# Kernel optimization log

Measured on AMD Instinct MI355X. Metric: run time of the kernel, lower is better.

## Reference

```python
import jax, jax.numpy as jnp
import numpy as np

# Config matching init_kwargs: input_shape=(C,T,H,W)=(512,32,14,14), window_size=9, n_heads=8
B, C, T, H, W = 2, 512, 32, 14, 14
N, K = 8, 9
CI = C // N              # per-head inter channels (64)
P = (K - 1) // 2         # symmetric temporal zero-pad so S == T


def setup_inputs() -> dict:
    key = jax.random.key(0)
    ks = jax.random.split(key, 7)
    s = 0.02
    return {
        "x":  jax.random.normal(ks[0], (B, C, T, H, W), jnp.float32),
        # per-head 1x1x1 conv (Linear3d) weights/biases, stacked over heads
        "Wq": jax.random.normal(ks[1], (N, CI, C), jnp.float32) * s,
        "bq": jax.random.normal(ks[2], (N, CI), jnp.float32) * s,
        "Wk": jax.random.normal(ks[3], (N, CI, C), jnp.float32) * s,
        "bk": jax.random.normal(ks[4], (N, CI), jnp.float32) * s,
        "Wv": jax.random.normal(ks[5], (N, CI, C), jnp.float32) * s,
        "bv": jax.random.normal(ks[6], (N, CI), jnp.float32) * s,
    }


def reference(x, Wq, bq, Wk, bk, Wv, bv):
    # x: (B, C, T, H, W). Dropout (p=0.25) is inference-mode identity.
    Bx, Cx, Tx, Hx, Wd = x.shape
    HW = Hx * Wd
    xf = x.reshape(Bx, Cx, Tx, HW)

    # Queries: every original frame is the center of its own window -> project x directly.
    q = jnp.einsum('bctp,nic->bnitp', xf, Wq) + bq[None, :, :, None, None]  # (B,N,ci,T,HW)

    # Keys/values on temporally zero-padded input (Pad3d gives S == T windows).
    xp = jnp.pad(xf, ((0, 0), (0, 0), (P, P), (0, 0)))  # (B,C,T+K-1,HW)
    k = jnp.einsum('bctp,nic->bnitp', xp, Wk) + bk[None, :, :, None, None]
    v = jnp.einsum('bctp,nic->bnitp', xp, Wv) + bv[None, :, :, None, None]

    # Sliding windows over padded time: window s covers padded frames s..s+K-1
    win = jnp.arange(Tx)[:, None] + jnp.arange(K)[None, :]  # (T,K)
    kw = k[:, :, :, win]  # (B,N,ci,T,K,HW)
    vw = v[:, :, :, win].reshape(Bx, N, CI, Tx, K * HW)

    # alpha[b,n,t,p,m] = sum_i q[b,n,i,t,p] * k_win[b,n,i,t,m]; softmax over keys m
    alpha = jnp.einsum('bnitp,bnitkm->bntpkm', q, kw).reshape(Bx, N, Tx, HW, K * HW)
    alpha = jax.nn.softmax(alpha, axis=-1)

    # y = alpha @ value -> (B,N,ci,T,HW); head concat is channel-major reshape
    y = jnp.einsum('bntpm,bnitm->bnitp', alpha, vw)
    z = y.reshape(Bx, Cx, Tx, Hx, Wd) + x  # residual
    return z
```

## Files before the change

### kernel.cpp

```cpp
#include <hip/hip_runtime.h>
#include <hip/hip_bf16.h>
#include <stdint.h>
#include <cstddef>

#define BB  2
#define CC  512
#define TT  32
#define HWP 196
#define NH  8
#define KWIN 9
#define CID 64
#define PPAD 4
#define TP  40
#define MTOT 12544
#define NTOT 1536
#define VSLOT 224
#define GPITCH 72
#define LOG2E 1.44269504f

typedef unsigned short u16;
typedef unsigned int   u32;
typedef __attribute__((ext_vector_type(8))) short short8;
typedef __attribute__((ext_vector_type(4))) float floatx4;

__device__ __forceinline__ u16 f2bf(float f) {
    u32 u = __float_as_uint(f);
    u32 r = (u + 0x7fffu + ((u >> 16) & 1u)) >> 16;
    return (u16)r;
}
__device__ __forceinline__ u32 pack2bf(float a, float b) {
    return (u32)f2bf(a) | ((u32)f2bf(b) << 16);
}
__device__ __forceinline__ u32 packtrunc(float a, float b) {
    return __builtin_amdgcn_perm(__float_as_uint(b), __float_as_uint(a), 0x07060302u);
}
__device__ __forceinline__ float fexp2(float x) {
    return __builtin_amdgcn_exp2f(x);
}

__global__ __launch_bounds__(256) void prep_misc(
    const float* __restrict__ Wq, const float* __restrict__ Wk,
    const float* __restrict__ Wv, u16* __restrict__ Wbf,
    const float* __restrict__ bk, const float* __restrict__ bv,
    u16* __restrict__ Kout, u16* __restrict__ Vtp)
{
    int id = blockIdx.x * 256 + threadIdx.x;
    const int wtot = NTOT * CC / 2;
    const int kper = 2 * NH * 8 * HWP * 32;
    const int vper = 2 * NH * 8 * 64 * (VSLOT/2);
    if (id < wtot) {
        int c2 = id & 255;
        int oc = id >> 8;
        int kind = oc >> 9;
        int idx = oc & 511;
        const float* src = (kind == 0 ? Wq : (kind == 1 ? Wk : Wv)) + (size_t)idx * CC + c2 * 2;
        ((u32*)Wbf)[id] = pack2bf(src[0], src[1]);
    } else if (id < wtot + kper) {
        int i = id - wtot;
        int ci2 = i & 31; i >>= 5;
        int p = i % HWP;  i /= HWP;
        int fr = i & 7;   i >>= 3;
        int head = i & 7;
        int b = i >> 3;
        int tp = fr < 4 ? fr : fr + 32;
        const float* bias = bk + head * CID + ci2 * 2;
        size_t addr = (((size_t)(b * NH + head) * TP + tp) * HWP + p) * 32 + ci2;
        ((u32*)Kout)[addr] = pack2bf(bias[0], bias[1]);
    } else if (id < wtot + kper + vper) {
        int i = id - wtot - kper;
        int s2 = i % (VSLOT/2); i /= (VSLOT/2);
        int ci = i & 63; i >>= 6;
        int fr = i & 7;  i >>= 3;
        int head = i & 7;
        int b = i >> 3;
        int tp = fr < 4 ? fr : fr + 32;
        float bias = bv[head * CID + ci];
        size_t addr = (((size_t)(b * NH + head) * TP + tp) * 64 + ci) * (VSLOT/2) + s2;
        ((u32*)Vtp)[addr] = pack2bf(bias, bias);
    }
}

__global__ __launch_bounds__(256) void transpose_x(
    const float* __restrict__ x, u16* __restrict__ xt)
{
    __shared__ float T[64 * 197];
    int bx = blockIdx.x;
    int ct = bx & 7; bx >>= 3;
    int t = bx & 31;
    int b = bx >> 5;
    int tid = threadIdx.x;
    const float* src = x + ((size_t)(b * CC + ct * 64) * TT + t) * HWP;
    for (int i = tid; i < 64 * HWP; i += 256) {
        int c = i / HWP;
        int p = i - c * HWP;
        T[c * 197 + p] = src[(size_t)c * (TT * HWP) + p];
    }
    __syncthreads();
    u16* dst = xt + (size_t)((b * TT + t) * HWP) * CC + ct * 64;
    for (int i = tid; i < HWP * 64; i += 256) {
        int p = i >> 6;
        int c = i & 63;
        dst[(size_t)p * CC + c] = f2bf(T[c * 197 + p]);
    }
}

__global__ __launch_bounds__(512) void proj_gemm2(
    const u16* __restrict__ xt, const u16* __restrict__ Wbf,
    const float* __restrict__ bq, const float* __restrict__ bk,
    const float* __restrict__ bv,
    u16* __restrict__ Qout, u16* __restrict__ Kout, u16* __restrict__ Vplain)
{
    __shared__ u16 sA[128 * GPITCH];
    __shared__ u16 sB[256 * GPITCH];

    int bx = blockIdx.x;
    int nb = bx % 6;
    int mt = bx / 6;
    int tid = threadIdx.x;
    int wave = tid >> 6, lane = tid & 63, quad = lane >> 4, l15 = lane & 15;
    int wm = wave >> 2, wn = wave & 3;
    int mbase = mt * 128 + wm * 64;
    int nbase = nb * 256 + wn * 64;

    floatx4 acc[4][4];
    #pragma unroll
    for (int ms = 0; ms < 4; ms++)
        #pragma unroll
        for (int ns = 0; ns < 4; ns++)
            acc[ms][ns] = (floatx4){0.f, 0.f, 0.f, 0.f};

    const u16* agbase = xt + (size_t)(mt * 128) * CC;
    const u16* bgbase = Wbf + (size_t)(nb * 256) * CC;

    for (int kc = 0; kc < 8; kc++) {
        __syncthreads();
        #pragma unroll
        for (int it = 0; it < 2; it++) {
            int idx = it * 512 + tid;
            int row = idx >> 3, jj = idx & 7;
            uint4 v = *(const uint4*)(agbase + (size_t)row * CC + kc * 64 + jj * 8);
            *(uint4*)&sA[row * GPITCH + jj * 8] = v;
        }
        #pragma unroll
        for (int it = 0; it < 4; it++) {
            int idx = it * 512 + tid;
            int row = idx >> 3, jj = idx & 7;
            uint4 v = *(const uint4*)(bgbase + (size_t)row * CC + kc * 64 + jj * 8);
            *(uint4*)&sB[row * GPITCH + jj * 8] = v;
        }
        __syncthreads();

        #pragma unroll
        for (int kk = 0; kk < 2; kk++) {
            short8 af[4], bf[4];
            #pragma unroll
            for (int ms = 0; ms < 4; ms++)
                af[ms] = *(const short8*)&sA[(wm * 64 + ms * 16 + l15) * GPITCH + kk * 32 + quad * 8];
            #pragma unroll
            for (int ns = 0; ns < 4; ns++)
                bf[ns] = *(const short8*)&sB[(wn * 64 + ns * 16 + l15) * GPITCH + kk * 32 + quad * 8];
            #pragma unroll
            for (int ms = 0; ms < 4; ms++)
                #pragma unroll
                for (int ns = 0; ns < 4; ns++)
                    acc[ms][ns] = __builtin_amdgcn_mfma_f32_16x16x32_bf16(
                        af[ms], bf[ns], acc[ms][ns], 0, 0, 0);
        }
    }

    float biasv[4];
    #pragma unroll
    for (int ns = 0; ns < 4; ns++) {
        int n = nbase + ns * 16 + l15;
        int kind = n >> 9;
        int idx = n & 511;
        const float* bpb = kind == 0 ? bq : (kind == 1 ? bk : bv);
        biasv[ns] = bpb[idx];
    }

    #pragma unroll
    for (int ms = 0; ms < 4; ms++) {
        #pragma unroll
        for (int r = 0; r < 4; r++) {
            int m = mbase + ms * 16 + quad * 4 + r;
            int b = m / (TT * HWP);
            int rem = m - b * (TT * HWP);
            int t = rem / HWP;
            int p = rem - t * HWP;
            #pragma unroll
            for (int ns = 0; ns < 4; ns++) {
                int n = nbase + ns * 16 + l15;
                int kind = n >> 9;
                int idx = n & 511;
                int head = idx >> 6;
                int ci = idx & 63;
                float val = acc[ms][ns][r] + biasv[ns];
                if (kind == 0) {
                    Qout[(((size_t)(b * NH + head) * TT + t) * HWP + p) * CID + ci]
                        = f2bf(val * LOG2E);
                } else if (kind == 1) {
                    Kout[(((size_t)(b * NH + head) * TP + (t + PPAD)) * HWP + p) * CID + ci]
                        = f2bf(val);
                } else {
                    Vplain[(((size_t)(b * NH + head) * TT + t) * HWP + p) * CID + ci]
                        = f2bf(val);
                }
            }
        }
    }
}

__global__ __launch_bounds__(256) void v_reformat(
    const u16* __restrict__ Vplain, u16* __restrict__ Vtp)
{
    __shared__ u16 T[HWP * 66];
    int bx = blockIdx.x;
    int t = bx & 31;
    int slab = bx >> 5;
    int tid = threadIdx.x;
    const u32* src = (const u32*)(Vplain + ((size_t)slab * TT + t) * (HWP * CID));
    for (int i = tid; i < HWP * 32; i += 256) {
        int p = i >> 5, c2 = i & 31;
        u32 v = src[i];
        T[p * 66 + c2 * 2]     = (u16)(v & 0xffffu);
        T[p * 66 + c2 * 2 + 1] = (u16)(v >> 16);
    }
    __syncthreads();
    u32* dst = (u32*)(Vtp + ((size_t)slab * TP + (t + PPAD)) * (64 * VSLOT));
    for (int i = tid; i < 64 * 98; i += 256) {
        int ci = i / 98;
        int s2 = i - ci * 98;
        int s = s2 * 2;
        int s5 = s & 31;
        int p0 = (s & ~31) | (((s5 >> 2) & 1) << 4) | ((s5 >> 3) << 2) | (s5 & 3);
        u32 lo = T[p0 * 66 + ci];
        u32 hi = T[(p0 + 1) * 66 + ci];
        dst[ci * (VSLOT / 2) + s2] = lo | (hi << 16);
    }
}

__global__ __launch_bounds__(256, 2) void attn_mfma4(
    const float* __restrict__ x,
    const u16* __restrict__ Qb, const u16* __restrict__ Kb,
    const u16* __restrict__ Vtp, float* __restrict__ zout)
{
    __shared__ float eT[HWP * 66];

    int i = blockIdx.x;
    int xcd = i & 7;
    int r = i >> 3;
    int slab = ((r >= 32) ? 8 : 0) | xcd;
    int t = r & 31;
    int b = slab >> 3, n = slab & 7;

    int tid = threadIdx.x;
    int wave = tid >> 6;
    int lane = tid & 63;
    int quad = lane >> 4, l15 = lane & 15;

    const u16* kfr0 = Kb + (size_t)slab * (TP * HWP) * CID;
    const u16* vslab = Vtp + (size_t)slab * (TP * 64 * VSLOT);
    const float tmask = (quad == 0) ? 1.0f : 0.0f;

    short8 qf[4][2];
    #pragma unroll
    for (int j = 0; j < 4; j++) {
        int qrow = (wave + 4 * j) * 16 + l15;
        qrow = qrow < HWP ? qrow : (HWP - 1);
        const u16* qp = Qb + ((size_t)(slab * TT + t) * HWP + qrow) * CID;
        qf[j][0] = *(const short8*)(qp + quad * 8);
        qf[j][1] = *(const short8*)(qp + 32 + quad * 8);
    }

    floatx4 acc[4][4];
    floatx4 accl[4];
    #pragma unroll
    for (int j = 0; j < 4; j++) {
        #pragma unroll
        for (int cg = 0; cg < 4; cg++) acc[j][cg] = (floatx4){0.f, 0.f, 0.f, 0.f};
        accl[j] = (floatx4){0.f, 0.f, 0.f, 0.f};
    }

    union { u32 w[4]; short8 s; } ones;
    ones.w[0] = 0x3F803F80u; ones.w[1] = 0x3F803F80u;
    ones.w[2] = 0x3F803F80u; ones.w[3] = 0x3F803F80u;

    #define KLOAD(c, D00, D01, D10, D11) do {                                    \
        const u16* a0_ = kfr0 + (size_t)(rbase + (c) * 32 + l15) * CID + quad * 8;\
        const u16* a1_ = a0_ + (size_t)16 * CID;                                 \
        D00 = *(const short8*)a0_;  D01 = *(const short8*)(a0_ + 32);            \
        D10 = *(const short8*)a1_;  D11 = *(const short8*)(a1_ + 32);            \
    } while (0)

    #define KLOADTAIL(D00, D01) do {                                             \
        int g_ = rbase + 192 + l15;                                              \
        g_ = g_ < (TP * HWP - 1) ? g_ : (TP * HWP - 1);                          \
        const u16* a0_ = kfr0 + (size_t)g_ * CID + quad * 8;                     \
        D00 = *(const short8*)a0_;  D01 = *(const short8*)(a0_ + 32);            \
    } while (0)

    #define VLOAD(c, D0, D1, D2, D3) do {                                        \
        const u16* v_ = vfr + l15 * VSLOT + (c) * 32 + quad * 8;                 \
        D0 = *(const short8*)v_;                                                 \
        D1 = *(const short8*)(v_ + 16 * VSLOT);                                  \
        D2 = *(const short8*)(v_ + 32 * VSLOT);                                  \
        D3 = *(const short8*)(v_ + 48 * VSLOT);                                  \
    } while (0)

    #define CHUNK_FULL(K00, K01, K10, K11, V0, V1, V2, V3)                       \
        _Pragma("unroll")                                                        \
        for (int j = 0; j < 4; j++) {                                            \
            floatx4 sc0 = (floatx4){0.f, 0.f, 0.f, 0.f};                         \
            sc0 = __builtin_amdgcn_mfma_f32_16x16x32_bf16(K00, qf[j][0], sc0, 0, 0, 0); \
            sc0 = __builtin_amdgcn_mfma_f32_16x16x32_bf16(K01, qf[j][1], sc0, 0, 0, 0); \
            floatx4 sc1 = (floatx4){0.f, 0.f, 0.f, 0.f};                         \
            sc1 = __builtin_amdgcn_mfma_f32_16x16x32_bf16(K10, qf[j][0], sc1, 0, 0, 0); \
            sc1 = __builtin_amdgcn_mfma_f32_16x16x32_bf16(K11, qf[j][1], sc1, 0, 0, 0); \
            union { u32 w[4]; short8 s; } pf;                                    \
            pf.w[0] = packtrunc(fexp2(sc0[0]), fexp2(sc0[1]));                   \
            pf.w[1] = packtrunc(fexp2(sc0[2]), fexp2(sc0[3]));                   \
            pf.w[2] = packtrunc(fexp2(sc1[0]), fexp2(sc1[1]));                   \
            pf.w[3] = packtrunc(fexp2(sc1[2]), fexp2(sc1[3]));                   \
            acc[j][0] = __builtin_amdgcn_mfma_f32_16x16x32_bf16(pf.s, V0, acc[j][0], 0, 0, 0); \
            acc[j][1] = __builtin_amdgcn_mfma_f32_16x16x32_bf16(pf.s, V1, acc[j][1], 0, 0, 0); \
            acc[j][2] = __builtin_amdgcn_mfma_f32_16x16x32_bf16(pf.s, V2, acc[j][2], 0, 0, 0); \
            acc[j][3] = __builtin_amdgcn_mfma_f32_16x16x32_bf16(pf.s, V3, acc[j][3], 0, 0, 0); \
            accl[j]   = __builtin_amdgcn_mfma_f32_16x16x32_bf16(pf.s, ones.s, accl[j], 0, 0, 0); \
        }

    #define CHUNK_TAIL(K00, K01, V0, V1, V2, V3)                                 \
        _Pragma("unroll")                                                        \
        for (int j = 0; j < 4; j++) {                                            \
            floatx4 sc0 = (floatx4){0.f, 0.f, 0.f, 0.f};                         \
            sc0 = __builtin_amdgcn_mfma_f32_16x16x32_bf16(K00, qf[j][0], sc0, 0, 0, 0); \
            sc0 = __builtin_amdgcn_mfma_f32_16x16x32_bf16(K01, qf[j][1], sc0, 0, 0, 0); \
            union { u32 w[4]; short8 s; } pf;                                    \
            pf.w[0] = packtrunc(fexp2(sc0[0]) * tmask, fexp2(sc0[1]) * tmask);   \
            pf.w[1] = packtrunc(fexp2(sc0[2]) * tmask, fexp2(sc0[3]) * tmask);   \
            pf.w[2] = 0u;                                                        \
            pf.w[3] = 0u;                                                        \
            acc[j][0] = __builtin_amdgcn_mfma_f32_16x16x32_bf16(pf.s, V0, acc[j][0], 0, 0, 0); \
            acc[j][1] = __builtin_amdgcn_mfma_f32_16x16x32_bf16(pf.s, V1, acc[j][1], 0, 0, 0); \
            acc[j][2] = __builtin_amdgcn_mfma_f32_16x16x32_bf16(pf.s, V2, acc[j][2], 0, 0, 0); \
            acc[j][3] = __builtin_amdgcn_mfma_f32_16x16x32_bf16(pf.s, V3, acc[j][3], 0, 0, 0); \
            accl[j]   = __builtin_amdgcn_mfma_f32_16x16x32_bf16(pf.s, ones.s, accl[j], 0, 0, 0); \
        }

    for (int f = 0; f < KWIN; f++) {
        int rbase = (t + f) * HWP;
        const u16* vfr = vslab + (size_t)(t + f) * (64 * VSLOT);

        short8 ka00, ka01, ka10, ka11, kb00, kb01, kb10, kb11;
        short8 va0, va1, va2, va3, vb0, vb1, vb2, vb3;

        KLOAD(0, ka00, ka01, ka10, ka11);  VLOAD(0, va0, va1, va2, va3);
        KLOAD(1, kb00, kb01, kb10, kb11);  VLOAD(1, vb0, vb1, vb2, vb3);
        CHUNK_FULL(ka00, ka01, ka10, ka11, va0, va1, va2, va3);
        KLOAD(2, ka00, ka01, ka10, ka11);  VLOAD(2, va0, va1, va2, va3);
        CHUNK_FULL(kb00, kb01, kb10, kb11, vb0, vb1, vb2, vb3);
        KLOAD(3, kb00, kb01, kb10, kb11);  VLOAD(3, vb0, vb1, vb2, vb3);
        CHUNK_FULL(ka00, ka01, ka10, ka11, va0, va1, va2, va3);
        KLOAD(4, ka00, ka01, ka10, ka11);  VLOAD(4, va0, va1, va2, va3);
        CHUNK_FULL(kb00, kb01, kb10, kb11, vb0, vb1, vb2, vb3);
        KLOAD(5, kb00, kb01, kb10, kb11);  VLOAD(5, vb0, vb1, vb2, vb3);
        CHUNK_FULL(ka00, ka01, ka10, ka11, va0, va1, va2, va3);
        KLOADTAIL(ka00, ka01);             VLOAD(6, va0, va1, va2, va3);
        CHUNK_FULL(kb00, kb01, kb10, kb11, vb0, vb1, vb2, vb3);
        CHUNK_TAIL(ka00, ka01, va0, va1, va2, va3);
    }

    #undef KLOAD
    #undef KLOADTAIL
    #undef VLOAD
    #undef CHUNK_FULL
    #undef CHUNK_TAIL

    #pragma unroll
    for (int j = 0; j < 4; j++) {
        int tg = wave + 4 * j;
        float il[4];
        #pragma unroll
        for (int rr = 0; rr < 4; rr++) il[rr] = 1.0f / accl[j][rr];
        #pragma unroll
        for (int cg = 0; cg < 4; cg++) {
            #pragma unroll
            for (int rr = 0; rr < 4; rr++) {
                int p = tg * 16 + quad * 4 + rr;
                if (p < HWP)
                    eT[p * 66 + cg * 16 + l15] = acc[j][cg][rr] * il[rr];
            }
        }
    }
    __syncthreads();

    if (tid < HWP) {
        size_t base = ((size_t)(b * CC + n * CID) * TT + t) * HWP + tid;
        for (int ci = 0; ci < 64; ci++) {
            size_t a = base + (size_t)ci * (TT * HWP);
            zout[a] = eT[tid * 66 + ci] + x[a];
        }
    }
}

extern "C" void kernel_launch(void* const* d_in, const int* in_sizes, int n_in,
                              void* d_out, int out_size, void* d_ws, size_t ws_size,
                              hipStream_t stream) {
    const float* x  = (const float*)d_in[0];
    const float* Wq = (const float*)d_in[1];
    const float* bq = (const float*)d_in[2];
    const float* Wk = (const float*)d_in[3];
    const float* bk = (const float*)d_in[4];
    const float* Wv = (const float*)d_in[5];
    const float* bv = (const float*)d_in[6];
    float* z = (float*)d_out;

    const size_t qElems   = (size_t)BB * NH * TT * HWP * CID;
    const size_t kElems   = (size_t)BB * NH * TP * HWP * CID;
    const size_t vtpElems = (size_t)BB * NH * TP * 64 * VSLOT;

    u16* Qw  = (u16*)d_ws;
    u16* Kw  = Qw + qElems;
    u16* Vtp = Kw + kElems;
    u16* Wb  = Vtp + vtpElems;
    u16* Xt  = (u16*)d_out;
    u16* Vpl = Xt + qElems;

    {
        const int wtot = NTOT * CC / 2;
        const int kper = 2 * NH * 8 * HWP * 32;
        const int vper = 2 * NH * 8 * 64 * (VSLOT / 2);
        prep_misc<<<(wtot + kper + vper + 255) / 256, 256, 0, stream>>>(
            Wq, Wk, Wv, Wb, bk, bv, Kw, Vtp);
    }
    transpose_x<<<BB * TT * 8, 256, 0, stream>>>(x, Xt);
    proj_gemm2<<<98 * 6, 512, 0, stream>>>(Xt, Wb, bq, bk, bv, Qw, Kw, Vpl);
    v_reformat<<<BB * NH * TT, 256, 0, stream>>>(Vpl, Vtp);
    attn_mfma4<<<512, 256, 0, stream>>>(x, Qw, Kw, Vtp, z);
}
```

Measured before the change: 254.5 us.

## Split attention query rows across two blocks and drop K/V double buffering

Each attention block now handles half of the 196 query positions (two 16-row tiles per wave instead of four), doubling the grid from 512 to 1024 blocks. The aim is better CU occupancy and lower per-thread register pressure. The manual ping-pong K/V register prefetch is replaced with a simple unrolled loop, and the output epilogue is spread across all 256 threads. In exchange, every K/V tile is now loaded by twice as many blocks, so K/V memory traffic doubles, and some load/compute overlap may be lost. The second half-block is partly wasted because 196 is not a multiple of 128.

After: 328.0 us. 28.9% more time.

```diff
diff --git a/kernel.cpp b/kernel.cpp
--- a/kernel.cpp
+++ b/kernel.cpp
@@ -244,13 +244,15 @@
     const u16* __restrict__ Qb, const u16* __restrict__ Kb,
     const u16* __restrict__ Vtp, float* __restrict__ zout)
 {
-    __shared__ float eT[HWP * 66];
+    __shared__ float eT[128 * 66];
 
     int i = blockIdx.x;
     int xcd = i & 7;
     int r = i >> 3;
-    int slab = ((r >= 32) ? 8 : 0) | xcd;
-    int t = r & 31;
+    int slab = ((r >= 64) ? 8 : 0) | xcd;
+    int rr = r & 63;
+    int t = rr >> 1;
+    int h = rr & 1;
     int b = slab >> 3, n = slab & 7;
 
     int tid = threadIdx.x;
@@ -262,20 +264,21 @@
     const u16* vslab = Vtp + (size_t)slab * (TP * 64 * VSLOT);
     const float tmask = (quad == 0) ? 1.0f : 0.0f;
 
-    short8 qf[4][2];
-    #pragma unroll
-    for (int j = 0; j < 4; j++) {
-        int qrow = (wave + 4 * j) * 16 + l15;
+    short8 qf[2][2];
+    #pragma unroll
+    for (int j = 0; j < 2; j++) {
+        int tg = 8 * h + wave + 4 * j;
+        int qrow = tg * 16 + l15;
         qrow = qrow < HWP ? qrow : (HWP - 1);
         const u16* qp = Qb + ((size_t)(slab * TT + t) * HWP + qrow) * CID;
         qf[j][0] = *(const short8*)(qp + quad * 8);
         qf[j][1] = *(const short8*)(qp + 32 + quad * 8);
     }
 
-    floatx4 acc[4][4];
-    floatx4 accl[4];
-    #pragma unroll
-    for (int j = 0; j < 4; j++) {
+    floatx4 acc[2][4];
+    floatx4 accl[2];
+    #pragma unroll
+    for (int j = 0; j < 2; j++) {
         #pragma unroll
         for (int cg = 0; cg < 4; cg++) acc[j][cg] = (floatx4){0.f, 0.f, 0.f, 0.f};
         accl[j] = (floatx4){0.f, 0.f, 0.f, 0.f};
@@ -309,7 +312,7 @@
 
     #define CHUNK_FULL(K00, K01, K10, K11, V0, V1, V2, V3)                       \
         _Pragma("unroll")                                                        \
-        for (int j = 0; j < 4; j++) {                                            \
+        for (int j = 0; j < 2; j++) {                                            \
             floatx4 sc0 = (floatx4){0.f, 0.f, 0.f, 0.f};                         \
             sc0 = __builtin_amdgcn_mfma_f32_16x16x32_bf16(K00, qf[j][0], sc0, 0, 0, 0); \
             sc0 = __builtin_amdgcn_mfma_f32_16x16x32_bf16(K01, qf[j][1], sc0, 0, 0, 0); \
@@ -330,7 +333,7 @@
 
     #define CHUNK_TAIL(K00, K01, V0, V1, V2, V3)                                 \
         _Pragma("unroll")                                                        \
-        for (int j = 0; j < 4; j++) {                                            \
+        for (int j = 0; j < 2; j++) {                                            \
             floatx4 sc0 = (floatx4){0.f, 0.f, 0.f, 0.f};                         \
             sc0 = __builtin_amdgcn_mfma_f32_16x16x32_bf16(K00, qf[j][0], sc0, 0, 0, 0); \
             sc0 = __builtin_amdgcn_mfma_f32_16x16x32_bf16(K01, qf[j][1], sc0, 0, 0, 0); \
@@ -350,23 +353,18 @@
         int rbase = (t + f) * HWP;
         const u16* vfr = vslab + (size_t)(t + f) * (64 * VSLOT);
 
-        short8 ka00, ka01, ka10, ka11, kb00, kb01, kb10, kb11;
-        short8 va0, va1, va2, va3, vb0, vb1, vb2, vb3;
-
-        KLOAD(0, ka00, ka01, ka10, ka11);  VLOAD(0, va0, va1, va2, va3);
-        KLOAD(1, kb00, kb01, kb10, kb11);  VLOAD(1, vb0, vb1, vb2, vb3);
-        CHUNK_FULL(ka00, ka01, ka10, ka11, va0, va1, va2, va3);
-        KLOAD(2, ka00, ka01, ka10, ka11);  VLOAD(2, va0, va1, va2, va3);
-        CHUNK_FULL(kb00, kb01, kb10, kb11, vb0, vb1, vb2, vb3);
-        KLOAD(3, kb00, kb01, kb10, kb11);  VLOAD(3, vb0, vb1, vb2, vb3);
-        CHUNK_FULL(ka00, ka01, ka10, ka11, va0, va1, va2, va3);
-        KLOAD(4, ka00, ka01, ka10, ka11);  VLOAD(4, va0, va1, va2, va3);
-        CHUNK_FULL(kb00, kb01, kb10, kb11, vb0, vb1, vb2, vb3);
-        KLOAD(5, kb00, kb01, kb10, kb11);  VLOAD(5, vb0, vb1, vb2, vb3);
-        CHUNK_FULL(ka00, ka01, ka10, ka11, va0, va1, va2, va3);
-        KLOADTAIL(ka00, ka01);             VLOAD(6, va0, va1, va2, va3);
-        CHUNK_FULL(kb00, kb01, kb10, kb11, vb0, vb1, vb2, vb3);
-        CHUNK_TAIL(ka00, ka01, va0, va1, va2, va3);
+        short8 k00, k01, k10, k11;
+        short8 v0, v1, v2, v3;
+
+        #pragma unroll
+        for (int c = 0; c < 6; c++) {
+            KLOAD(c, k00, k01, k10, k11);
+            VLOAD(c, v0, v1, v2, v3);
+            CHUNK_FULL(k00, k01, k10, k11, v0, v1, v2, v3);
+        }
+        KLOADTAIL(k00, k01);
+        VLOAD(6, v0, v1, v2, v3);
+        CHUNK_TAIL(k00, k01, v0, v1, v2, v3);
     }
 
     #undef KLOAD
@@ -376,28 +374,33 @@
     #undef CHUNK_TAIL
 
     #pragma unroll
-    for (int j = 0; j < 4; j++) {
-        int tg = wave + 4 * j;
+    for (int j = 0; j < 2; j++) {
+        int tg = 8 * h + wave + 4 * j;
         float il[4];
         #pragma unroll
-        for (int rr = 0; rr < 4; rr++) il[rr] = 1.0f / accl[j][rr];
+        for (int rr2 = 0; rr2 < 4; rr2++) il[rr2] = 1.0f / accl[j][rr2];
         #pragma unroll
         for (int cg = 0; cg < 4; cg++) {
             #pragma unroll
-            for (int rr = 0; rr < 4; rr++) {
-                int p = tg * 16 + quad * 4 + rr;
+            for (int rr2 = 0; rr2 < 4; rr2++) {
+                int p = tg * 16 + quad * 4 + rr2;
                 if (p < HWP)
-                    eT[p * 66 + cg * 16 + l15] = acc[j][cg][rr] * il[rr];
+                    eT[(p - 128 * h) * 66 + cg * 16 + l15] = acc[j][cg][rr2] * il[rr2];
             }
         }
     }
     __syncthreads();
 
-    if (tid < HWP) {
-        size_t base = ((size_t)(b * CC + n * CID) * TT + t) * HWP + tid;
-        for (int ci = 0; ci < 64; ci++) {
-            size_t a = base + (size_t)ci * (TT * HWP);
-            zout[a] = eT[tid * 66 + ci] + x[a];
+    {
+        int prow = tid >> 1;
+        int p = 128 * h + prow;
+        int ch = tid & 1;
+        if (p < HWP) {
+            size_t base = ((size_t)(b * CC + n * CID + ch * 32) * TT + t) * HWP + p;
+            for (int ci = 0; ci < 32; ci++) {
+                size_t a = base + (size_t)ci * (TT * HWP);
+                zout[a] = eT[prow * 66 + ch * 32 + ci] + x[a];
+            }
         }
     }
 }
@@ -435,5 +438,5 @@
     transpose_x<<<BB * TT * 8, 256, 0, stream>>>(x, Xt);
     proj_gemm2<<<98 * 6, 512, 0, stream>>>(Xt, Wb, bq, bk, bv, Qw, Kw, Vpl);
     v_reformat<<<BB * NH * TT, 256, 0, stream>>>(Vpl, Vtp);
-    attn_mfma4<<<512, 256, 0, stream>>>(x, Qw, Kw, Vtp, z);
-}
+    attn_mfma4<<<1024, 256, 0, stream>>>(x, Qw, Kw, Vtp, z);
+}
```
